# Kernel tuning notes

Measured on AMD Instinct MI355X. Metric: run time of the kernel, lower is better.

The kernel has to match this reference:

```python
import jax, jax.numpy as jnp
import numpy as np

EPS = 1e-07
NUM_HEADS = 8


def setup_inputs() -> dict:
    key = jax.random.key(0)
    ks = jax.random.split(key, 5)
    b, h, w, d = 16, 64, 64, 384
    return {
        "x_in": jax.random.normal(ks[0], (b, h, w, d), dtype=jnp.float32),
        "w_qkv": jax.random.normal(ks[1], (3 * d, d), dtype=jnp.float32) * 0.02,
        "b_qkv": jax.random.normal(ks[2], (3 * d,), dtype=jnp.float32) * 0.02,
        "w_proj": jax.random.normal(ks[3], (d, d), dtype=jnp.float32) * 0.02,
        "b_proj": jax.random.normal(ks[4], (d,), dtype=jnp.float32) * 0.02,
    }


def reference(x_in, w_qkv, b_qkv, w_proj, b_proj):
    b, h, w, d = x_in.shape
    n = h * w
    dh = d // NUM_HEADS
    x = x_in.reshape(b, n, d)
    # qkv projection: [b, n, 3d] -> [3, b, heads, n, dh]
    qkv = (x @ w_qkv.T + b_qkv).reshape(b, n, 3, NUM_HEADS, dh)
    qkv = jnp.transpose(qkv, (2, 0, 3, 1, 4))
    q, k, v = qkv[0], qkv[1], qkv[2]
    # softmax over the token (n) axis
    q = jax.nn.softmax(q, axis=-2)
    k = jax.nn.softmax(k, axis=-2)
    # linear attention: kv = K^T V  [b, heads, dh, dh]
    kt = jnp.swapaxes(k, -2, -1)
    kv = kt @ v
    num = q @ kv                                      # [b, heads, n, dh]
    denom = q @ jnp.sum(kt, axis=-1, keepdims=True) + EPS  # [b, heads, n, 1]
    attn = num / denom
    # merge heads -> [b, n, d]
    attn = jnp.swapaxes(attn, 1, 2).reshape(b, n, d)
    out = (attn @ w_proj.T + b_proj).reshape(b, h, w, d)
    return out
```

## Files before the change

kernel.cpp:

```cpp
#include <hip/hip_runtime.h>
#include <stdint.h>

typedef unsigned short u16;
typedef __bf16 bf16x8 __attribute__((ext_vector_type(8)));
typedef unsigned short u16x8 __attribute__((ext_vector_type(8)));
typedef float f32x4 __attribute__((ext_vector_type(4)));

#define BATCH 16
#define NTOK 4096
#define DMODEL 384
#define NHEAD 8
#define DH 48
#define M_ROWS 65536
#define QKVC 1152

static __device__ __forceinline__ float b2f(u16 u) {
    union { float f; unsigned int i; } x; x.i = ((unsigned int)u) << 16; return x.f;
}
static __device__ __forceinline__ u16 f2b(float f) {
    union { float f; unsigned int i; } x; x.f = f;
    unsigned int i = x.i;
    unsigned int r = (i + 0x7FFFu + ((i >> 16) & 1u)) >> 16;
    return (u16)r;
}

static __device__ __forceinline__ void gload_lds16(const void* g, void* l) {
    __builtin_amdgcn_global_load_lds(
        (const __attribute__((address_space(1))) void*)g,
        (__attribute__((address_space(3))) void*)l, 16, 0, 0);
}

__global__ __launch_bounds__(256) void cvt_f32_bf16(const float* __restrict__ src,
                                                    u16* __restrict__ dst, int n4) {
    int i = blockIdx.x * 256 + threadIdx.x;
    if (i < n4) {
        float4 v = ((const float4*)src)[i];
        ushort4 o;
        o.x = f2b(v.x); o.y = f2b(v.y); o.z = f2b(v.z); o.w = f2b(v.w);
        ((ushort4*)dst)[i] = o;
    }
}

template<bool OUTF32>
__global__ __launch_bounds__(256) void gemm_bt(const u16* __restrict__ A,
                                               const u16* __restrict__ B,
                                               const float* __restrict__ bias,
                                               void* __restrict__ Cout,
                                               int M, int N, int K) {
    __shared__ u16 As[128 * 32];
    __shared__ u16 Bs[128 * 32];
    const int tid  = threadIdx.x;
    const int lane = tid & 63;
    const int wave = tid >> 6;
    const int wr = wave >> 1, wc = wave & 1;
    const int fr = lane & 15;
    const int fk = (lane >> 4) * 8;
    const int m0 = blockIdx.y * 128, n0 = blockIdx.x * 128;
    const int ar = tid >> 2;
    const int ak = (tid & 3) * 8;

    f32x4 acc[4][4] = {};

    for (int kt = 0; kt < K; kt += 32) {
        gload_lds16(A + (size_t)(m0 + ar) * K + kt + ak,      As + tid * 8);
        gload_lds16(A + (size_t)(m0 + 64 + ar) * K + kt + ak, As + 2048 + tid * 8);
        gload_lds16(B + (size_t)(n0 + ar) * K + kt + ak,      Bs + tid * 8);
        gload_lds16(B + (size_t)(n0 + 64 + ar) * K + kt + ak, Bs + 2048 + tid * 8);
        __syncthreads();
        bf16x8 af[4], bfv[4];
        #pragma unroll
        for (int m = 0; m < 4; m++)
            af[m] = *(const bf16x8*)&As[(wr * 64 + m * 16 + fr) * 32 + fk];
        #pragma unroll
        for (int n = 0; n < 4; n++)
            bfv[n] = *(const bf16x8*)&Bs[(wc * 64 + n * 16 + fr) * 32 + fk];
        #pragma unroll
        for (int m = 0; m < 4; m++)
            #pragma unroll
            for (int n = 0; n < 4; n++)
                acc[m][n] = __builtin_amdgcn_mfma_f32_16x16x32_bf16(
                                af[m], bfv[n], acc[m][n], 0, 0, 0);
        __syncthreads();
    }
    const int orow = (lane >> 4) * 4;
    const int ocol = lane & 15;
    #pragma unroll
    for (int m = 0; m < 4; m++) {
        #pragma unroll
        for (int n = 0; n < 4; n++) {
            int col = n0 + wc * 64 + n * 16 + ocol;
            float bv = bias[col];
            #pragma unroll
            for (int j = 0; j < 4; j++) {
                int row = m0 + wr * 64 + m * 16 + orow + j;
                float v = acc[m][n][j] + bv;
                if constexpr (OUTF32)
                    ((float*)Cout)[(size_t)row * N + col] = v;
                else
                    ((u16*)Cout)[(size_t)row * N + col] = f2b(v);
            }
        }
    }
}

__global__ __launch_bounds__(256) void colstats(const u16* __restrict__ qkv,
                                                float2* __restrict__ part) {
    const int rc = blockIdx.x;
    const int cc = blockIdx.y;
    const int b  = blockIdx.z;
    const int col = cc * 256 + threadIdx.x;
    const u16* p = qkv + (size_t)(b * NTOK + rc * 256) * QKVC + col;
    float m0 = -1e30f, m1 = -1e30f, m2 = -1e30f, m3 = -1e30f;
    float s0 = 0.f, s1 = 0.f, s2 = 0.f, s3 = 0.f;
    for (int r = 0; r < 256; r += 4) {
        float v0 = b2f(p[(size_t)(r + 0) * QKVC]);
        float v1 = b2f(p[(size_t)(r + 1) * QKVC]);
        float v2 = b2f(p[(size_t)(r + 2) * QKVC]);
        float v3 = b2f(p[(size_t)(r + 3) * QKVC]);
        float n0 = fmaxf(m0, v0); s0 = s0 * __expf(m0 - n0) + __expf(v0 - n0); m0 = n0;
        float n1 = fmaxf(m1, v1); s1 = s1 * __expf(m1 - n1) + __expf(v1 - n1); m1 = n1;
        float n2 = fmaxf(m2, v2); s2 = s2 * __expf(m2 - n2) + __expf(v2 - n2); m2 = n2;
        float n3 = fmaxf(m3, v3); s3 = s3 * __expf(m3 - n3) + __expf(v3 - n3); m3 = n3;
    }
    float m = fmaxf(fmaxf(m0, m1), fmaxf(m2, m3));
    float s = s0 * __expf(m0 - m) + s1 * __expf(m1 - m)
            + s2 * __expf(m2 - m) + s3 * __expf(m3 - m);
    part[(((size_t)b * 3 + cc) * 16 + rc) * 256 + threadIdx.x] = make_float2(m, s);
}

__global__ __launch_bounds__(256) void colstats_reduce(const float2* __restrict__ part,
                                                       float2* __restrict__ stats) {
    int idx = blockIdx.x * 256 + threadIdx.x;
    int b = idx / 768, col = idx % 768;
    int cc = col >> 8, t = col & 255;
    const float2* pp = part + (((size_t)b * 3 + cc) * 16) * 256 + t;
    float m = -1e30f;
    #pragma unroll
    for (int r = 0; r < 16; r++) m = fmaxf(m, pp[r * 256].x);
    float s = 0.f;
    #pragma unroll
    for (int r = 0; r < 16; r++) { float2 v = pp[r * 256]; s += v.y * __expf(v.x - m); }
    stats[idx] = make_float2(m, 1.0f / s);
}

__global__ __launch_bounds__(256) void kv_accum_mfma(const u16* __restrict__ qkv,
                                                     const float2* __restrict__ stats,
                                                     float* __restrict__ kvt) {
    const int tc = blockIdx.x;
    const int h  = blockIdx.y;
    const int b  = blockIdx.z;
    __shared__ char ckv[96 * 256];
    __shared__ float km[48], ki[48];
    const int tid  = threadIdx.x;
    const int lane = tid & 63, wave = tid >> 6;
    const int fr = lane & 15, kg = lane >> 4;
    if (tid < 48) {
        float2 st = stats[b * 768 + 384 + h * 48 + tid];
        km[tid] = st.x; ki[tid] = st.y;
    }
    __syncthreads();
    f32x4 acc[3][3] = {};
    const size_t rowbase = (size_t)(b * NTOK + tc * 512);
    for (int iter = 0; iter < 4; iter++) {
        const size_t tbase = rowbase + iter * 128;
        for (int u = tid; u < 1536; u += 256) {
            int p = u / 24, c4 = u % 24;
            int t = p * 2;
            int kpart = (c4 < 12);
            int lch = kpart ? c4 * 4 : (c4 - 12) * 4;
            int ch  = kpart ? lch : (48 + lch);
            int gch = kpart ? (384 + h * 48 + lch) : (768 + h * 48 + lch);
            const u16* r0 = qkv + (tbase + t) * QKVC + gch;
            ushort4 a  = *(const ushort4*)r0;
            ushort4 bb = *(const ushort4*)(r0 + QKVC);
            #pragma unroll
            for (int e = 0; e < 4; e++) {
                u16 ae = ((const u16*)&a)[e], be = ((const u16*)&bb)[e];
                u16 lo, hi;
                if (kpart) {
                    float mm = km[lch + e], si = ki[lch + e];
                    lo = f2b(__expf(b2f(ae) - mm) * si);
                    hi = f2b(__expf(b2f(be) - mm) * si);
                } else { lo = ae; hi = be; }
                int che = ch + e;
                int byteoff = che * 256 + ((((t >> 3) ^ (che & 15)) << 4)) + ((t & 7) * 2);
                *(unsigned int*)(ckv + byteoff) = (unsigned int)lo | ((unsigned int)hi << 16);
            }
        }
        __syncthreads();
        const int g0 = wave * 4;
        bf16x8 afv[3], bfk[3];
        #pragma unroll
        for (int mt = 0; mt < 3; mt++) {
            int chv = 48 + mt * 16 + fr;
            afv[mt] = *(const bf16x8*)(ckv + chv * 256 + (((g0 + kg) ^ (chv & 15)) << 4));
            int chk = mt * 16 + fr;
            bfk[mt] = *(const bf16x8*)(ckv + chk * 256 + (((g0 + kg) ^ (chk & 15)) << 4));
        }
        #pragma unroll
        for (int mt = 0; mt < 3; mt++)
            #pragma unroll
            for (int nt = 0; nt < 3; nt++)
                acc[mt][nt] = __builtin_amdgcn_mfma_f32_16x16x32_bf16(
                                  afv[mt], bfk[nt], acc[mt][nt], 0, 0, 0);
        __syncthreads();
    }
    float* kp = kvt + (size_t)(b * NHEAD + h) * 2304;
    const int orow = kg * 4, ocol = fr;
    #pragma unroll
    for (int mt = 0; mt < 3; mt++)
        #pragma unroll
        for (int nt = 0; nt < 3; nt++)
            #pragma unroll
            for (int j = 0; j < 4; j++)
                atomicAdd(&kp[(mt * 16 + orow + j) * 48 + nt * 16 + ocol], acc[mt][nt][j]);
}

__global__ __launch_bounds__(256) void kvt_to_bf16(const float* __restrict__ kvt,
                                                   u16* __restrict__ kvtb) {
    int idx = blockIdx.x * 256 + threadIdx.x;
    int g  = idx / 3072;
    int r  = (idx >> 6) % 48;
    int ii = idx & 63;
    float v = (ii < 48) ? kvt[(size_t)g * 2304 + r * 48 + ii] : 0.f;
    kvtb[idx] = f2b(v);
}

__global__ __launch_bounds__(256) void attn_mfma(const u16* __restrict__ qkv,
                                                 const float2* __restrict__ stats,
                                                 const u16* __restrict__ kvtb,
                                                 u16* __restrict__ attnb) {
    const int tc = blockIdx.x;
    const int h  = blockIdx.y;
    const int b  = blockIdx.z;
    __shared__ u16 obuf[256][50];
    const int tid  = threadIdx.x;
    const int lane = tid & 63, wave = tid >> 6;
    const int fr = lane & 15, kg = lane >> 4;
    const int g = b * NHEAD + h;

    bf16x8 bf[3][2];
    #pragma unroll
    for (int nt = 0; nt < 3; nt++)
        #pragma unroll
        for (int kt = 0; kt < 2; kt++)
            bf[nt][kt] = *(const bf16x8*)(kvtb + (size_t)g * 3072 + (nt * 16 + fr) * 64
                                          + kt * 32 + kg * 8);
    float qm8[2][8], qi8[2][8];
    #pragma unroll
    for (int kt = 0; kt < 2; kt++) {
        int ch0 = kt * 32 + kg * 8;
        if (ch0 < 48) {
            #pragma unroll
            for (int e = 0; e < 8; e++) {
                float2 st = stats[b * 768 + h * 48 + ch0 + e];
                qm8[kt][e] = st.x; qi8[kt][e] = st.y;
            }
        }
    }

    f32x4 acc[4][3] = {};
    float den4[4];
    const size_t qbase = ((size_t)(b * NTOK + tc * 256 + wave * 64)) * QKVC + h * 48;
    #pragma unroll
    for (int m = 0; m < 4; m++) {
        const u16* qrow = qkv + qbase + (size_t)(m * 16 + fr) * QKVC;
        float denp = 0.f;
        bf16x8 af[2];
        #pragma unroll
        for (int kt = 0; kt < 2; kt++) {
            int ch0 = kt * 32 + kg * 8;
            u16x8 av = {};
            if (ch0 < 48) {
                ushort4 a0 = *(const ushort4*)(qrow + ch0);
                ushort4 a1 = *(const ushort4*)(qrow + ch0 + 4);
                #pragma unroll
                for (int e = 0; e < 8; e++) {
                    u16 qv = (e < 4) ? ((const u16*)&a0)[e] : ((const u16*)&a1)[e - 4];
                    float s = __expf(b2f(qv) - qm8[kt][e]) * qi8[kt][e];
                    denp += s;
                    av[e] = f2b(s);
                }
            }
            union { u16x8 u; bf16x8 b; } cvt; cvt.u = av;
            af[kt] = cvt.b;
        }
        denp += __shfl_xor(denp, 16);
        denp += __shfl_xor(denp, 32);
        den4[m] = denp + 1e-7f;
        #pragma unroll
        for (int nt = 0; nt < 3; nt++)
            #pragma unroll
            for (int kt = 0; kt < 2; kt++)
                acc[m][nt] = __builtin_amdgcn_mfma_f32_16x16x32_bf16(
                                 af[kt], bf[nt][kt], acc[m][nt], 0, 0, 0);
    }
    const int orow = kg * 4, ocol = fr;
    #pragma unroll
    for (int m = 0; m < 4; m++) {
        float rd[4];
        #pragma unroll
        for (int j = 0; j < 4; j++)
            rd[j] = 1.0f / __shfl(den4[m], orow + j);
        #pragma unroll
        for (int nt = 0; nt < 3; nt++)
            #pragma unroll
            for (int j = 0; j < 4; j++)
                obuf[wave * 64 + m * 16 + orow + j][nt * 16 + ocol] =
                    f2b(acc[m][nt][j] * rd[j]);
    }
    __syncthreads();
    u16* ob = attnb + ((size_t)(b * NTOK + tc * 256)) * DMODEL + h * 48;
    for (int u = tid; u < 6144; u += 256) {
        int t = u / 24, c2 = (u % 24) * 2;
        *(ushort2*)(ob + (size_t)t * DMODEL + c2) = *(const ushort2*)&obuf[t][c2];
    }
}

extern "C" void kernel_launch(void* const* d_in, const int* in_sizes, int n_in,
                              void* d_out, int out_size, void* d_ws, size_t ws_size,
                              hipStream_t stream) {
    const float* x     = (const float*)d_in[0];
    const float* wqkv  = (const float*)d_in[1];
    const float* bqkv  = (const float*)d_in[2];
    const float* wproj = (const float*)d_in[3];
    const float* bproj = (const float*)d_in[4];

    char* ws = (char*)d_ws;
    size_t off = 0;
    auto take = [&](size_t bytes) {
        char* p = ws + off;
        off = (off + bytes + 255) & ~(size_t)255;
        return p;
    };
    u16*    xb    = (u16*)take((size_t)M_ROWS * DMODEL * 2);
    u16*    wqb   = (u16*)take((size_t)QKVC * DMODEL * 2);
    u16*    wpb   = (u16*)take((size_t)DMODEL * DMODEL * 2);
    u16*    qkvb  = (u16*)take((size_t)M_ROWS * QKVC * 2);
    float2* stats = (float2*)take((size_t)BATCH * 768 * sizeof(float2));
    float2* part  = (float2*)take((size_t)BATCH * 3 * 16 * 256 * sizeof(float2));
    float*  kvt   = (float*)take((size_t)BATCH * NHEAD * DH * DH * sizeof(float));
    u16*    kvtb  = (u16*)take((size_t)BATCH * NHEAD * DH * 64 * 2);
    u16*    attnb = xb;

    cvt_f32_bf16<<<dim3(M_ROWS * DMODEL / 4 / 256), 256, 0, stream>>>(x, xb, M_ROWS * DMODEL / 4);
    cvt_f32_bf16<<<dim3(QKVC * DMODEL / 4 / 256), 256, 0, stream>>>(wqkv, wqb, QKVC * DMODEL / 4);
    cvt_f32_bf16<<<dim3(DMODEL * DMODEL / 4 / 256), 256, 0, stream>>>(wproj, wpb, DMODEL * DMODEL / 4);

    gemm_bt<false><<<dim3(QKVC / 128, M_ROWS / 128), 256, 0, stream>>>(
        xb, wqb, bqkv, qkvb, M_ROWS, QKVC, DMODEL);

    colstats<<<dim3(16, 3, BATCH), 256, 0, stream>>>(qkvb, part);
    colstats_reduce<<<dim3(BATCH * 768 / 256), 256, 0, stream>>>(part, stats);

    hipMemsetAsync(kvt, 0, (size_t)BATCH * NHEAD * DH * DH * sizeof(float), stream);
    kv_accum_mfma<<<dim3(NTOK / 512, NHEAD, BATCH), 256, 0, stream>>>(qkvb, stats, kvt);
    kvt_to_bf16<<<dim3(BATCH * NHEAD * DH * 64 / 256), 256, 0, stream>>>(kvt, kvtb);

    attn_mfma<<<dim3(16, NHEAD, BATCH), 256, 0, stream>>>(qkvb, stats, kvtb, attnb);

    gemm_bt<true><<<dim3(DMODEL / 128, M_ROWS / 128), 256, 0, stream>>>(
        attnb, wpb, bproj, d_out, M_ROWS, DMODEL, DMODEL);
}
```

Before: 427.0 us.

## Fuse softmax column sums into QKV GEMM epilogue and store head-major panels

The QKV GEMM epilogue now writes Q/K/V into per-(batch, which, head) contiguous panels of 4096x48 and accumulates exp() column sums with atomics. This replaces the separate colstats and reduce kernels, and it drops max subtraction, relying on small activations to avoid overflow. Workgroup IDs are remapped across XCDs to improve L2 locality. Downstream kernels read the contiguous panels, which should give better coalescing than the strided reads of the 1152-wide rows. The risks are exp overflow without the max shift, atomic contention, and strided 2-byte epilogue stores.

```diff
diff --git a/kernel.cpp b/kernel.cpp
--- a/kernel.cpp
+++ b/kernel.cpp
@@ -13,6 +13,7 @@
 #define DH 48
 #define M_ROWS 65536
 #define QKVC 1152
+#define HPANE (NTOK * DH)
 
 static __device__ __forceinline__ float b2f(u16 u) {
     union { float f; unsigned int i; } x; x.i = ((unsigned int)u) << 16; return x.f;
@@ -41,11 +42,12 @@
     }
 }
 
-template<bool OUTF32>
+template<bool OUTF32, bool QKV>
 __global__ __launch_bounds__(256) void gemm_bt(const u16* __restrict__ A,
                                                const u16* __restrict__ B,
                                                const float* __restrict__ bias,
                                                void* __restrict__ Cout,
+                                               float* __restrict__ statsOut,
                                                int M, int N, int K) {
     __shared__ u16 As[128 * 32];
     __shared__ u16 Bs[128 * 32];
@@ -55,7 +57,15 @@
     const int wr = wave >> 1, wc = wave & 1;
     const int fr = lane & 15;
     const int fk = (lane >> 4) * 8;
-    const int m0 = blockIdx.y * 128, n0 = blockIdx.x * 128;
+
+    const int nwg  = gridDim.x * gridDim.y;
+    const int orig = blockIdx.y * gridDim.x + blockIdx.x;
+    const int qq = nwg >> 3, rr = nwg & 7;
+    const int xcd = orig & 7, ii = orig >> 3;
+    const int wgid = (xcd < rr ? xcd * (qq + 1) : rr * (qq + 1) + (xcd - rr) * qq) + ii;
+    const int m0 = (wgid / gridDim.x) * 128;
+    const int n0 = (wgid % gridDim.x) * 128;
+
     const int ar = tid >> 2;
     const int ak = (tid & 3) * 8;
 
@@ -84,103 +94,99 @@
     }
     const int orow = (lane >> 4) * 4;
     const int ocol = lane & 15;
-    #pragma unroll
-    for (int m = 0; m < 4; m++) {
+
+    if constexpr (QKV) {
+        const int bb   = m0 >> 12;
+        const int tok0 = (m0 & 4095) + wr * 64 + orow;
+        float colsum[4] = {0.f, 0.f, 0.f, 0.f};
         #pragma unroll
         for (int n = 0; n < 4; n++) {
-            int col = n0 + wc * 64 + n * 16 + ocol;
-            float bv = bias[col];
-            #pragma unroll
-            for (int j = 0; j < 4; j++) {
-                int row = m0 + wr * 64 + m * 16 + orow + j;
-                float v = acc[m][n][j] + bv;
-                if constexpr (OUTF32)
-                    ((float*)Cout)[(size_t)row * N + col] = v;
-                else
-                    ((u16*)Cout)[(size_t)row * N + col] = f2b(v);
-            }
-        }
-    }
-}
-
-__global__ __launch_bounds__(256) void colstats(const u16* __restrict__ qkv,
-                                                float2* __restrict__ part) {
-    const int rc = blockIdx.x;
-    const int cc = blockIdx.y;
-    const int b  = blockIdx.z;
-    const int col = cc * 256 + threadIdx.x;
-    const u16* p = qkv + (size_t)(b * NTOK + rc * 256) * QKVC + col;
-    float m0 = -1e30f, m1 = -1e30f, m2 = -1e30f, m3 = -1e30f;
-    float s0 = 0.f, s1 = 0.f, s2 = 0.f, s3 = 0.f;
-    for (int r = 0; r < 256; r += 4) {
-        float v0 = b2f(p[(size_t)(r + 0) * QKVC]);
-        float v1 = b2f(p[(size_t)(r + 1) * QKVC]);
-        float v2 = b2f(p[(size_t)(r + 2) * QKVC]);
-        float v3 = b2f(p[(size_t)(r + 3) * QKVC]);
-        float n0 = fmaxf(m0, v0); s0 = s0 * __expf(m0 - n0) + __expf(v0 - n0); m0 = n0;
-        float n1 = fmaxf(m1, v1); s1 = s1 * __expf(m1 - n1) + __expf(v1 - n1); m1 = n1;
-        float n2 = fmaxf(m2, v2); s2 = s2 * __expf(m2 - n2) + __expf(v2 - n2); m2 = n2;
-        float n3 = fmaxf(m3, v3); s3 = s3 * __expf(m3 - n3) + __expf(v3 - n3); m3 = n3;
-    }
-    float m = fmaxf(fmaxf(m0, m1), fmaxf(m2, m3));
-    float s = s0 * __expf(m0 - m) + s1 * __expf(m1 - m)
-            + s2 * __expf(m2 - m) + s3 * __expf(m3 - m);
-    part[(((size_t)b * 3 + cc) * 16 + rc) * 256 + threadIdx.x] = make_float2(m, s);
-}
-
-__global__ __launch_bounds__(256) void colstats_reduce(const float2* __restrict__ part,
-                                                       float2* __restrict__ stats) {
-    int idx = blockIdx.x * 256 + threadIdx.x;
-    int b = idx / 768, col = idx % 768;
-    int cc = col >> 8, t = col & 255;
-    const float2* pp = part + (((size_t)b * 3 + cc) * 16) * 256 + t;
-    float m = -1e30f;
-    #pragma unroll
-    for (int r = 0; r < 16; r++) m = fmaxf(m, pp[r * 256].x);
-    float s = 0.f;
-    #pragma unroll
-    for (int r = 0; r < 16; r++) { float2 v = pp[r * 256]; s += v.y * __expf(v.x - m); }
-    stats[idx] = make_float2(m, 1.0f / s);
+            const int cbase = n0 + wc * 64 + n * 16;
+            const int which = cbase / 384;
+            const int hh  = (cbase - which * 384) / 48;
+            const int dh0 = cbase - which * 384 - hh * 48;
+            u16* dst = (u16*)Cout + ((size_t)((bb * 3 + which) * 8 + hh)) * HPANE
+                       + dh0 + ocol;
+            const float bv = bias[cbase + ocol];
+            const bool qk = (cbase < 768);
+            #pragma unroll
+            for (int m = 0; m < 4; m++) {
+                #pragma unroll
+                for (int j = 0; j < 4; j++) {
+                    float v = acc[m][n][j] + bv;
+                    u16 vb = f2b(v);
+                    dst[(size_t)(tok0 + m * 16 + j) * 48] = vb;
+                    if (qk) colsum[n] += __expf(b2f(vb));
+                }
+            }
+        }
+        #pragma unroll
+        for (int n = 0; n < 4; n++) {
+            const int cbase = n0 + wc * 64 + n * 16;
+            if (cbase < 768) {
+                float s = colsum[n];
+                s += __shfl_xor(s, 16);
+                s += __shfl_xor(s, 32);
+                if (lane < 16)
+                    atomicAdd(&statsOut[bb * 768 + cbase + ocol], s);
+            }
+        }
+    } else {
+        #pragma unroll
+        for (int m = 0; m < 4; m++) {
+            #pragma unroll
+            for (int n = 0; n < 4; n++) {
+                int col = n0 + wc * 64 + n * 16 + ocol;
+                float bv = bias[col];
+                #pragma unroll
+                for (int j = 0; j < 4; j++) {
+                    int row = m0 + wr * 64 + m * 16 + orow + j;
+                    float v = acc[m][n][j] + bv;
+                    if constexpr (OUTF32)
+                        ((float*)Cout)[(size_t)row * N + col] = v;
+                    else
+                        ((u16*)Cout)[(size_t)row * N + col] = f2b(v);
+                }
+            }
+        }
+    }
 }
 
 __global__ __launch_bounds__(256) void kv_accum_mfma(const u16* __restrict__ qkv,
-                                                     const float2* __restrict__ stats,
+                                                     const float* __restrict__ stats,
                                                      float* __restrict__ kvt) {
     const int tc = blockIdx.x;
     const int h  = blockIdx.y;
     const int b  = blockIdx.z;
     __shared__ char ckv[96 * 256];
-    __shared__ float km[48], ki[48];
+    __shared__ float ki[48];
     const int tid  = threadIdx.x;
     const int lane = tid & 63, wave = tid >> 6;
     const int fr = lane & 15, kg = lane >> 4;
-    if (tid < 48) {
-        float2 st = stats[b * 768 + 384 + h * 48 + tid];
-        km[tid] = st.x; ki[tid] = st.y;
-    }
+    if (tid < 48) ki[tid] = 1.0f / stats[b * 768 + 384 + h * 48 + tid];
     __syncthreads();
     f32x4 acc[3][3] = {};
-    const size_t rowbase = (size_t)(b * NTOK + tc * 512);
+    const u16* kpan = qkv + ((size_t)(b * 3 + 1) * 8 + h) * HPANE;
+    const u16* vpan = qkv + ((size_t)(b * 3 + 2) * 8 + h) * HPANE;
     for (int iter = 0; iter < 4; iter++) {
-        const size_t tbase = rowbase + iter * 128;
+        const size_t tbase = (size_t)(tc * 512 + iter * 128);
         for (int u = tid; u < 1536; u += 256) {
             int p = u / 24, c4 = u % 24;
             int t = p * 2;
             int kpart = (c4 < 12);
             int lch = kpart ? c4 * 4 : (c4 - 12) * 4;
             int ch  = kpart ? lch : (48 + lch);
-            int gch = kpart ? (384 + h * 48 + lch) : (768 + h * 48 + lch);
-            const u16* r0 = qkv + (tbase + t) * QKVC + gch;
+            const u16* r0 = (kpart ? kpan : vpan) + (tbase + t) * 48 + lch;
             ushort4 a  = *(const ushort4*)r0;
-            ushort4 bb = *(const ushort4*)(r0 + QKVC);
+            ushort4 bb = *(const ushort4*)(r0 + 48);
             #pragma unroll
             for (int e = 0; e < 4; e++) {
                 u16 ae = ((const u16*)&a)[e], be = ((const u16*)&bb)[e];
                 u16 lo, hi;
                 if (kpart) {
-                    float mm = km[lch + e], si = ki[lch + e];
-                    lo = f2b(__expf(b2f(ae) - mm) * si);
-                    hi = f2b(__expf(b2f(be) - mm) * si);
+                    float si = ki[lch + e];
+                    lo = f2b(__expf(b2f(ae)) * si);
+                    hi = f2b(__expf(b2f(be)) * si);
                 } else { lo = ae; hi = be; }
                 int che = ch + e;
                 int byteoff = che * 256 + ((((t >> 3) ^ (che & 15)) << 4)) + ((t & 7) * 2);
@@ -227,7 +233,7 @@
 }
 
 __global__ __launch_bounds__(256) void attn_mfma(const u16* __restrict__ qkv,
-                                                 const float2* __restrict__ stats,
+                                                 const float* __restrict__ stats,
                                                  const u16* __restrict__ kvtb,
                                                  u16* __restrict__ attnb) {
     const int tc = blockIdx.x;
@@ -246,25 +252,22 @@
         for (int kt = 0; kt < 2; kt++)
             bf[nt][kt] = *(const bf16x8*)(kvtb + (size_t)g * 3072 + (nt * 16 + fr) * 64
                                           + kt * 32 + kg * 8);
-    float qm8[2][8], qi8[2][8];
+    float qi8[2][8];
     #pragma unroll
     for (int kt = 0; kt < 2; kt++) {
         int ch0 = kt * 32 + kg * 8;
-        if (ch0 < 48) {
-            #pragma unroll
-            for (int e = 0; e < 8; e++) {
-                float2 st = stats[b * 768 + h * 48 + ch0 + e];
-                qm8[kt][e] = st.x; qi8[kt][e] = st.y;
-            }
-        }
-    }
-
+        if (ch0 < 48)
+            #pragma unroll
+            for (int e = 0; e < 8; e++)
+                qi8[kt][e] = 1.0f / stats[b * 768 + h * 48 + ch0 + e];
+    }
+
+    const u16* qpan = qkv + ((size_t)(b * 3 + 0) * 8 + h) * HPANE;
     f32x4 acc[4][3] = {};
     float den4[4];
-    const size_t qbase = ((size_t)(b * NTOK + tc * 256 + wave * 64)) * QKVC + h * 48;
     #pragma unroll
     for (int m = 0; m < 4; m++) {
-        const u16* qrow = qkv + qbase + (size_t)(m * 16 + fr) * QKVC;
+        const u16* qrow = qpan + (size_t)(tc * 256 + wave * 64 + m * 16 + fr) * 48;
         float denp = 0.f;
         bf16x8 af[2];
         #pragma unroll
@@ -277,7 +280,7 @@
                 #pragma unroll
                 for (int e = 0; e < 8; e++) {
                     u16 qv = (e < 4) ? ((const u16*)&a0)[e] : ((const u16*)&a1)[e - 4];
-                    float s = __expf(b2f(qv) - qm8[kt][e]) * qi8[kt][e];
+                    float s = __expf(b2f(qv)) * qi8[kt][e];
                     denp += s;
                     av[e] = f2b(s);
                 }
@@ -333,32 +336,30 @@
         off = (off + bytes + 255) & ~(size_t)255;
         return p;
     };
-    u16*    xb    = (u16*)take((size_t)M_ROWS * DMODEL * 2);
-    u16*    wqb   = (u16*)take((size_t)QKVC * DMODEL * 2);
-    u16*    wpb   = (u16*)take((size_t)DMODEL * DMODEL * 2);
-    u16*    qkvb  = (u16*)take((size_t)M_ROWS * QKVC * 2);
-    float2* stats = (float2*)take((size_t)BATCH * 768 * sizeof(float2));
-    float2* part  = (float2*)take((size_t)BATCH * 3 * 16 * 256 * sizeof(float2));
-    float*  kvt   = (float*)take((size_t)BATCH * NHEAD * DH * DH * sizeof(float));
-    u16*    kvtb  = (u16*)take((size_t)BATCH * NHEAD * DH * 64 * 2);
-    u16*    attnb = xb;
+    u16*   xb    = (u16*)take((size_t)M_ROWS * DMODEL * 2);
+    u16*   wqb   = (u16*)take((size_t)QKVC * DMODEL * 2);
+    u16*   wpb   = (u16*)take((size_t)DMODEL * DMODEL * 2);
+    u16*   qkvb  = (u16*)take((size_t)M_ROWS * QKVC * 2);
+    float* stats = (float*)take((size_t)BATCH * 768 * sizeof(float));
+    float* kvt   = (float*)take((size_t)BATCH * NHEAD * DH * DH * sizeof(float));
+    u16*   kvtb  = (u16*)take((size_t)BATCH * NHEAD * DH * 64 * 2);
+    u16*   attnb = xb;
 
     cvt_f32_bf16<<<dim3(M_ROWS * DMODEL / 4 / 256), 256, 0, stream>>>(x, xb, M_ROWS * DMODEL / 4);
     cvt_f32_bf16<<<dim3(QKVC * DMODEL / 4 / 256), 256, 0, stream>>>(wqkv, wqb, QKVC * DMODEL / 4);
     cvt_f32_bf16<<<dim3(DMODEL * DMODEL / 4 / 256), 256, 0, stream>>>(wproj, wpb, DMODEL * DMODEL / 4);
 
-    gemm_bt<false><<<dim3(QKVC / 128, M_ROWS / 128), 256, 0, stream>>>(
-        xb, wqb, bqkv, qkvb, M_ROWS, QKVC, DMODEL);
-
-    colstats<<<dim3(16, 3, BATCH), 256, 0, stream>>>(qkvb, part);
-    colstats_reduce<<<dim3(BATCH * 768 / 256), 256, 0, stream>>>(part, stats);
-
+    hipMemsetAsync(stats, 0, (size_t)BATCH * 768 * sizeof(float), stream);
     hipMemsetAsync(kvt, 0, (size_t)BATCH * NHEAD * DH * DH * sizeof(float), stream);
+
+    gemm_bt<false, true><<<dim3(QKVC / 128, M_ROWS / 128), 256, 0, stream>>>(
+        xb, wqb, bqkv, qkvb, stats, M_ROWS, QKVC, DMODEL);
+
     kv_accum_mfma<<<dim3(NTOK / 512, NHEAD, BATCH), 256, 0, stream>>>(qkvb, stats, kvt);
     kvt_to_bf16<<<dim3(BATCH * NHEAD * DH * 64 / 256), 256, 0, stream>>>(kvt, kvtb);
 
     attn_mfma<<<dim3(16, NHEAD, BATCH), 256, 0, stream>>>(qkvb, stats, kvtb, attnb);
 
-    gemm_bt<true><<<dim3(DMODEL / 128, M_ROWS / 128), 256, 0, stream>>>(
-        attnb, wpb, bproj, d_out, M_ROWS, DMODEL, DMODEL);
-}
+    gemm_bt<true, false><<<dim3(DMODEL / 128, M_ROWS / 128), 256, 0, stream>>>(
+        attnb, wpb, bproj, d_out, nullptr, M_ROWS, DMODEL, DMODEL);
+}
```

Result: faster. 400.3 us (-6.3%).
